# Kernel optimization log

Measured on AMD Instinct MI355X. Metric: run time of the kernel, lower is better.

Reference implementation:

```python
import jax, jax.numpy as jnp
import numpy as np

B, T, C, H, W = 4, 5, 512, 32, 32   # bt = B*T = 20
G = 32                              # GroupNorm groups
EPS = 1e-6


def group_norm(x, gamma, beta):
    # x: [N, C, H, W]; normalize per (group-channels, H, W)
    n, c, h, w = x.shape
    xg = x.reshape(n, G, c // G, h * w)
    mu = jnp.mean(xg, axis=(2, 3), keepdims=True)
    var = jnp.mean((xg - mu) ** 2, axis=(2, 3), keepdims=True)
    xn = ((xg - mu) * jax.lax.rsqrt(var + EPS)).reshape(n, c, h, w)
    return xn * gamma[None, :, None, None] + beta[None, :, None, None]


def conv1x1(x, w, b):
    # 1x1 conv == channel matmul. x: [N,C,H,W], w: [O,C], b: [O]
    return jnp.einsum('nchw,oc->nohw', x, w) + b[None, :, None, None]


def setup_inputs() -> dict:
    key = jax.random.key(0)
    ks = jax.random.split(key, 9)
    inp = {'x': jax.random.normal(ks[0], (B * T, C, H, W), jnp.float32)}
    for i, nm in enumerate(['wq', 'wk', 'wv', 'wo', 'wqt', 'wkt', 'wvt', 'wot']):
        inp[nm] = jax.random.normal(ks[i + 1], (C, C), jnp.float32) * 0.02
        inp['b' + nm[1:]] = jnp.zeros((C,), jnp.float32)
    inp['gamma_s'] = jnp.ones((C,), jnp.float32)
    inp['beta_s'] = jnp.zeros((C,), jnp.float32)
    inp['gamma_t'] = jnp.ones((C,), jnp.float32)
    inp['beta_t'] = jnp.zeros((C,), jnp.float32)
    return inp


def reference(x, wq, bq, wk, bk, wv, bv, wo, bo,
              wqt, bqt, wkt, bkt, wvt, bvt, wot, bot,
              gamma_s, beta_s, gamma_t, beta_t):
    scale = float(C) ** -0.5

    # ---- spatial attention (AttnBlock.forward) ----
    hn = group_norm(x, gamma_s, beta_s)
    q = conv1x1(hn, wq, bq).reshape(B * T, C, H * W)
    k = conv1x1(hn, wk, bk).reshape(B * T, C, H * W)
    v = conv1x1(hn, wv, bv).reshape(B * T, C, H * W)
    # scores [bt, hw_q, hw_k], softmax over keys
    att = jax.nn.softmax(jnp.einsum('bcq,bck->bqk', q, k) * scale, axis=2)
    hsp = jnp.einsum('bck,bqk->bcq', v, att).reshape(B * T, C, H, W)
    spatio = x + conv1x1(hsp, wo, bo)

    # ---- temporal attention across t=5 frames per pixel ----
    hn = group_norm(spatio, gamma_t, beta_t)
    q5 = conv1x1(hn, wqt, bqt).reshape(B, T, C, H, W)
    k5 = conv1x1(hn, wkt, bkt).reshape(B, T, C, H, W)
    v5 = conv1x1(hn, wvt, bvt).reshape(B, T, C, H, W)
    # per-pixel [t, t] attention, softmax over key-frame axis s
    att_t = jax.nn.softmax(jnp.einsum('btchw,bschw->bhwts', q5, k5) * scale, axis=-1)
    htp = jnp.einsum('bhwts,bschw->btchw', att_t, v5).reshape(B * T, C, H, W)

    # NOTE: residual is the ORIGINAL x (faithful to the source), not spatio
    return x + conv1x1(htp, wot, bot)
```

## Files before the change

### kernel.cpp

```cpp
#include <hip/hip_runtime.h>
#include <hip/hip_bf16.h>
#include <stdint.h>

typedef unsigned short u16;
typedef __attribute__((ext_vector_type(8))) short bf16x8;
typedef __attribute__((ext_vector_type(4))) float f32x4;

#define DI __device__ __forceinline__

DI float b2f(u16 u) { return __uint_as_float(((uint32_t)u) << 16); }
DI u16 f2b(float f) {
  uint32_t u = __float_as_uint(f);
  u += 0x7fff + ((u >> 16) & 1);
  return (u16)(u >> 16);
}

DI void gld_lds16(const u16* g, u16* l) {
  __builtin_amdgcn_global_load_lds((const __attribute__((address_space(1))) void*)g,
                                   (__attribute__((address_space(3))) void*)l,
                                   16, 0, 0);
}

__global__ __launch_bounds__(256)
void setup_wb(const float* __restrict__ w0, const float* __restrict__ w1,
              const float* __restrict__ w2, const float* __restrict__ w3,
              const float* __restrict__ w4, const float* __restrict__ w5,
              const float* __restrict__ w6, const float* __restrict__ w7,
              const float* __restrict__ b0, const float* __restrict__ b1,
              const float* __restrict__ b2, const float* __restrict__ b3,
              const float* __restrict__ b4, const float* __restrict__ b5,
              const float* __restrict__ b6, const float* __restrict__ b7,
              u16* __restrict__ dst, float* __restrict__ bdst)
{
  if (blockIdx.x >= 1024) {
    const float* bs[8] = {b0, b1, b2, b3, b4, b5, b6, b7};
    const int a = blockIdx.x - 1024;
    const int i = threadIdx.x;
    bdst[a * 512 + i] = bs[a][i];
    bdst[a * 512 + i + 256] = bs[a][i + 256];
    return;
  }
  const float* srcs[8] = {w0, w1, w2, w3, w4, w5, w6, w7};
  const int mat = blockIdx.x >> 7;
  const int i = (((blockIdx.x & 127) << 8) + threadIdx.x) * 8;
  const float* s = srcs[mat];
  float4 a = *(const float4*)(s + i);
  float4 b = *(const float4*)(s + i + 4);
  alignas(16) u16 v[8] = {f2b(a.x), f2b(a.y), f2b(a.z), f2b(a.w),
                          f2b(b.x), f2b(b.y), f2b(b.z), f2b(b.w)};
  *(uint4*)(dst + (long)mat * 262144 + i) = *(const uint4*)v;
}

template<int OUTF32, int BIASMODE, int RESID>
__global__ __launch_bounds__(512, 2)
void gemm256(const u16* __restrict__ A, long sA, long lda,
             const u16* __restrict__ B, long sB, long ldb,
             void* __restrict__ C, long sC,
             const float* __restrict__ bias,
             const float* __restrict__ resid, long sR,
             int N, int K, float alpha)
{
  __shared__ u16 lA[4 * 8192];
  __shared__ u16 lB[4 * 8192];
  const int t = threadIdx.x;
  const int lane = t & 63, wid = t >> 6;
  const int wr = wid >> 2, wc = wid & 3;
  const int ml = lane & 15, qd = lane >> 4;

  const int nx = gridDim.x;
  const int bid = blockIdx.y * nx + blockIdx.x;
  const int nper = (nx * gridDim.y) >> 3;
  const int nid = (bid & 7) * nper + (bid >> 3);
  const int m0 = (nid / nx) * 256, n0 = (nid % nx) * 256;

  const long bz = blockIdx.z;
  const u16* Ab = A + bz * sA;
  const u16* Bb = B + bz * sB;

  const int sw = ((lane & 3) ^ ((lane >> 3) & 3)) << 3;
  const int srow = wid * 32 + (lane >> 2);
  const u16* ApS = Ab + (long)(m0 + srow) * lda + sw;
  const u16* BpS = Bb + (long)(n0 + srow) * ldb + sw;
  u16* lwA = lA + wid * 1024;
  u16* lwB = lB + wid * 1024;

  f32x4 acc[8][4];
#pragma unroll
  for (int i = 0; i < 8; ++i)
#pragma unroll
    for (int j = 0; j < 4; ++j) acc[i][j] = (f32x4){0.f, 0.f, 0.f, 0.f};

  const int NT = K >> 5;

  auto stageA = [&](int tk) {
    const int bo = (tk & 3) << 13;
    const u16* p = ApS + ((long)tk << 5);
    gld_lds16(p,              lwA + bo);
    gld_lds16(p + (lda << 4), lwA + bo + 512);
  };
  auto stageB = [&](int tk) {
    const int bo = (tk & 3) << 13;
    const u16* p = BpS + ((long)tk << 5);
    gld_lds16(p,              lwB + bo);
    gld_lds16(p + (ldb << 4), lwB + bo + 512);
  };

  const int koff = (qd ^ ((ml >> 1) & 3)) << 3;
  const int rAo = (wr * 128 + ml) * 32 + koff;
  const int rBo = (wc * 64 + ml) * 32 + koff;

  stageA(0); stageB(0); stageA(1); stageB(1); stageA(2); stageB(2);
  asm volatile("s_waitcnt vmcnt(8)" ::: "memory");
  __builtin_amdgcn_s_barrier();
  __builtin_amdgcn_sched_barrier(0);

  for (int tk = 0; tk < NT; ++tk) {
    const int bo = (tk & 3) << 13;
    const u16* pa = lA + bo + rAo;
    const u16* pb = lB + bo + rBo;
    bf16x8 bfr[4], af[4];

#pragma unroll
    for (int n = 0; n < 4; ++n) bfr[n] = *(const bf16x8*)(pb + n * 512);
#pragma unroll
    for (int m = 0; m < 4; ++m) af[m] = *(const bf16x8*)(pa + m * 512);
    if (tk + 3 < NT) stageA(tk + 3);
    __builtin_amdgcn_sched_barrier(0);
    __builtin_amdgcn_s_barrier();
    asm volatile("s_waitcnt lgkmcnt(0)" ::: "memory");
    __builtin_amdgcn_sched_barrier(0);
    __builtin_amdgcn_s_setprio(1);
#pragma unroll
    for (int m = 0; m < 4; ++m)
#pragma unroll
      for (int n = 0; n < 4; ++n)
        acc[m][n] = __builtin_amdgcn_mfma_f32_16x16x32_bf16(af[m], bfr[n], acc[m][n], 0, 0, 0);
    __builtin_amdgcn_s_setprio(0);
    __builtin_amdgcn_sched_barrier(0);
    __builtin_amdgcn_s_barrier();
    __builtin_amdgcn_sched_barrier(0);

#pragma unroll
    for (int m = 0; m < 4; ++m) af[m] = *(const bf16x8*)(pa + (m + 4) * 512);
    if (tk + 3 < NT) stageB(tk + 3);
    __builtin_amdgcn_sched_barrier(0);
    __builtin_amdgcn_s_barrier();
    asm volatile("s_waitcnt lgkmcnt(0)" ::: "memory");
    __builtin_amdgcn_sched_barrier(0);
    __builtin_amdgcn_s_setprio(1);
#pragma unroll
    for (int m = 0; m < 4; ++m)
#pragma unroll
      for (int n = 0; n < 4; ++n)
        acc[m + 4][n] = __builtin_amdgcn_mfma_f32_16x16x32_bf16(af[m], bfr[n], acc[m + 4][n], 0, 0, 0);
    __builtin_amdgcn_s_setprio(0);
    __builtin_amdgcn_sched_barrier(0);

    if (tk < NT - 1) {
      const int rem = NT - 2 - tk;
      if (rem >= 2)      asm volatile("s_waitcnt vmcnt(8)" ::: "memory");
      else if (rem == 1) asm volatile("s_waitcnt vmcnt(4)" ::: "memory");
      else               asm volatile("s_waitcnt vmcnt(0)" ::: "memory");
      __builtin_amdgcn_s_barrier();
      __builtin_amdgcn_sched_barrier(0);
    }
  }

  const long cb = bz * sC;
#pragma unroll
  for (int mt = 0; mt < 8; ++mt) {
#pragma unroll
    for (int nt = 0; nt < 4; ++nt) {
#pragma unroll
      for (int r = 0; r < 4; ++r) {
        int rr = m0 + wr * 128 + mt * 16 + qd * 4 + r;
        int cc = n0 + wc * 64 + nt * 16 + ml;
        float v = acc[mt][nt][r] * alpha;
        if (BIASMODE == 1) v += bias[rr];
        if (BIASMODE == 2) v += bias[cc];
        long idx = (long)rr * N + cc;
        if (RESID) v += resid[bz * sR + idx];
        if (OUTF32) ((float*)C)[cb + idx] = v;
        else        ((u16*)C)[cb + idx] = f2b(v);
      }
    }
  }
}

__global__ __launch_bounds__(256)
void groupnorm_f32(const float* __restrict__ x, const float* __restrict__ gamma,
                   const float* __restrict__ beta, u16* __restrict__ out)
{
  const int C = 512, HW = 1024;
  const int n = blockIdx.x >> 5, g = blockIdx.x & 31;
  const float* xg = x + ((long)n * C + g * 16) * HW;
  const int t = threadIdx.x;
  float s = 0.f, ss = 0.f;
  for (int ch = t; ch < 4096; ch += 256) {
    float4 u = *(const float4*)(xg + ch * 4);
    s += u.x + u.y + u.z + u.w;
    ss += u.x * u.x + u.y * u.y + u.z * u.z + u.w * u.w;
  }
#pragma unroll
  for (int off = 32; off > 0; off >>= 1) { s += __shfl_xor(s, off); ss += __shfl_xor(ss, off); }
  __shared__ float rs[4], rss[4];
  if ((t & 63) == 0) { rs[t >> 6] = s; rss[t >> 6] = ss; }
  __syncthreads();
  s  = rs[0] + rs[1] + rs[2] + rs[3];
  ss = rss[0] + rss[1] + rss[2] + rss[3];
  const float mu = s * (1.f / 16384.f);
  const float var = ss * (1.f / 16384.f) - mu * mu;
  const float rstd = rsqrtf(var + 1e-6f);
  float gm[16], bt[16];
#pragma unroll
  for (int i = 0; i < 16; ++i) {
    float ga = gamma[g * 16 + i];
    gm[i] = ga * rstd;
    bt[i] = beta[g * 16 + i] - mu * ga * rstd;
  }
  for (int p = t; p < 1024; p += 256) {
    alignas(16) u16 vals[16];
#pragma unroll
    for (int i = 0; i < 16; ++i)
      vals[i] = f2b(xg[(long)i * HW + p] * gm[i] + bt[i]);
    u16* dst = out + ((long)n * HW + p) * C + g * 16;
    *(uint4*)dst       = *(const uint4*)&vals[0];
    *(uint4*)(dst + 8) = *(const uint4*)&vals[8];
  }
}

__global__ __launch_bounds__(256)
void groupnorm_bf16(const u16* __restrict__ x, const float* __restrict__ gamma,
                    const float* __restrict__ beta, u16* __restrict__ out)
{
  const int C = 512, HW = 1024;
  const int n = blockIdx.x >> 5, g = blockIdx.x & 31;
  const u16* xg = x + ((long)n * C + g * 16) * HW;
  const int t = threadIdx.x;
  float s = 0.f, ss = 0.f;
  for (int ch = t; ch < 2048; ch += 256) {
    uint4 u = *(const uint4*)(xg + ch * 8);
    uint32_t w[4] = {u.x, u.y, u.z, u.w};
#pragma unroll
    for (int k = 0; k < 4; ++k) {
      float f0 = __uint_as_float(w[k] << 16);
      float f1 = __uint_as_float(w[k] & 0xffff0000u);
      s += f0 + f1; ss += f0 * f0 + f1 * f1;
    }
  }
#pragma unroll
  for (int off = 32; off > 0; off >>= 1) { s += __shfl_xor(s, off); ss += __shfl_xor(ss, off); }
  __shared__ float rs[4], rss[4];
  if ((t & 63) == 0) { rs[t >> 6] = s; rss[t >> 6] = ss; }
  __syncthreads();
  s  = rs[0] + rs[1] + rs[2] + rs[3];
  ss = rss[0] + rss[1] + rss[2] + rss[3];
  const float mu = s * (1.f / 16384.f);
  const float var = ss * (1.f / 16384.f) - mu * mu;
  const float rstd = rsqrtf(var + 1e-6f);
  float gm[16], bt[16];
#pragma unroll
  for (int i = 0; i < 16; ++i) {
    float ga = gamma[g * 16 + i];
    gm[i] = ga * rstd;
    bt[i] = beta[g * 16 + i] - mu * ga * rstd;
  }
  for (int p = t; p < 1024; p += 256) {
    alignas(16) u16 vals[16];
#pragma unroll
    for (int i = 0; i < 16; ++i)
      vals[i] = f2b(b2f(xg[(long)i * HW + p]) * gm[i] + bt[i]);
    u16* dst = out + ((long)n * HW + p) * C + g * 16;
    *(uint4*)dst       = *(const uint4*)&vals[0];
    *(uint4*)(dst + 8) = *(const uint4*)&vals[8];
  }
}

__global__ __launch_bounds__(256)
void softmax1024(u16* __restrict__ data)
{
  u16* row = data + (long)blockIdx.x * 1024;
  const int t = threadIdx.x;
  uint2 u = *(const uint2*)(row + t * 4);
  float v[4];
  v[0] = __uint_as_float(u.x << 16); v[1] = __uint_as_float(u.x & 0xffff0000u);
  v[2] = __uint_as_float(u.y << 16); v[3] = __uint_as_float(u.y & 0xffff0000u);
  float mx = fmaxf(fmaxf(v[0], v[1]), fmaxf(v[2], v[3]));
#pragma unroll
  for (int off = 32; off > 0; off >>= 1) mx = fmaxf(mx, __shfl_xor(mx, off));
  __shared__ float red[8];
  if ((t & 63) == 0) red[t >> 6] = mx;
  __syncthreads();
  mx = fmaxf(fmaxf(red[0], red[1]), fmaxf(red[2], red[3]));
  float e[4]; float s = 0.f;
#pragma unroll
  for (int k = 0; k < 4; ++k) { e[k] = __expf(v[k] - mx); s += e[k]; }
#pragma unroll
  for (int off = 32; off > 0; off >>= 1) s += __shfl_xor(s, off);
  if ((t & 63) == 0) red[4 + (t >> 6)] = s;
  __syncthreads();
  s = red[4] + red[5] + red[6] + red[7];
  float inv = 1.f / s;
  uint2 o;
  o.x = (uint32_t)f2b(e[0] * inv) | ((uint32_t)f2b(e[1] * inv) << 16);
  o.y = (uint32_t)f2b(e[2] * inv) | ((uint32_t)f2b(e[3] * inv) << 16);
  *(uint2*)(row + t * 4) = o;
}

__global__ __launch_bounds__(256)
void temporal_attn(const u16* __restrict__ qkv, u16* __restrict__ htp)
{
  const int t = threadIdx.x;
  const int wv = t >> 6, lane = t & 63;
  const int pix = blockIdx.x * 4 + wv;
  const int b = pix >> 10, p = pix & 1023;
  const long fs = 1024l * 1536;
  const long rowbase = ((long)b * 5 * 1024 + p) * 1536 + lane * 8;

  float qf[5][8], kf[5][8];
#pragma unroll
  for (int f = 0; f < 5; ++f) {
    bf16x8 qv = *(const bf16x8*)(qkv + rowbase + f * fs);
    bf16x8 kv = *(const bf16x8*)(qkv + rowbase + f * fs + 512);
#pragma unroll
    for (int u = 0; u < 8; ++u) { qf[f][u] = b2f((u16)qv[u]); kf[f][u] = b2f((u16)kv[u]); }
  }
  float sc[25];
#pragma unroll
  for (int i = 0; i < 5; ++i)
#pragma unroll
    for (int j = 0; j < 5; ++j) {
      float a = 0.f;
#pragma unroll
      for (int u = 0; u < 8; ++u) a += qf[i][u] * kf[j][u];
      sc[i * 5 + j] = a;
    }
#pragma unroll
  for (int m = 1; m < 64; m <<= 1)
#pragma unroll
    for (int s = 0; s < 25; ++s) sc[s] += __shfl_xor(sc[s], m);

  const float scale = 0.04419417382415922f;
  float att[5][5];
#pragma unroll
  for (int i = 0; i < 5; ++i) {
    float m = sc[i * 5];
#pragma unroll
    for (int j = 1; j < 5; ++j) m = fmaxf(m, sc[i * 5 + j]);
    float ssum = 0.f;
#pragma unroll
    for (int j = 0; j < 5; ++j) { att[i][j] = __expf((sc[i * 5 + j] - m) * scale); ssum += att[i][j]; }
    float inv = 1.f / ssum;
#pragma unroll
    for (int j = 0; j < 5; ++j) att[i][j] *= inv;
  }

  float of[5][8];
#pragma unroll
  for (int i = 0; i < 5; ++i)
#pragma unroll
    for (int u = 0; u < 8; ++u) of[i][u] = 0.f;
#pragma unroll
  for (int s = 0; s < 5; ++s) {
    bf16x8 vvv = *(const bf16x8*)(qkv + rowbase + s * fs + 1024);
#pragma unroll
    for (int u = 0; u < 8; ++u) {
      float vf = b2f((u16)vvv[u]);
#pragma unroll
      for (int i = 0; i < 5; ++i) of[i][u] += att[i][s] * vf;
    }
  }
  const long obase = ((long)b * 5 * 1024 + p) * 512 + lane * 8;
#pragma unroll
  for (int i = 0; i < 5; ++i) {
    alignas(16) u16 ob[8];
#pragma unroll
    for (int u = 0; u < 8; ++u) ob[u] = f2b(of[i][u]);
    *(uint4*)(htp + obase + i * 1024 * 512) = *(const uint4*)ob;
  }
}

extern "C" void kernel_launch(void* const* d_in, const int* in_sizes, int n_in,
                              void* d_out, int out_size, void* d_ws, size_t ws_size,
                              hipStream_t stream)
{
  const float* x   = (const float*)d_in[0];
  const float* wq  = (const float*)d_in[1];
  const float* bq  = (const float*)d_in[2];
  const float* wk  = (const float*)d_in[3];
  const float* bk  = (const float*)d_in[4];
  const float* wv  = (const float*)d_in[5];
  const float* bv  = (const float*)d_in[6];
  const float* wo  = (const float*)d_in[7];
  const float* bo  = (const float*)d_in[8];
  const float* wqt = (const float*)d_in[9];
  const float* bqt = (const float*)d_in[10];
  const float* wkt = (const float*)d_in[11];
  const float* bkt = (const float*)d_in[12];
  const float* wvt = (const float*)d_in[13];
  const float* bvt = (const float*)d_in[14];
  const float* wot = (const float*)d_in[15];
  const float* bot = (const float*)d_in[16];
  const float* gs  = (const float*)d_in[17];
  const float* bs  = (const float*)d_in[18];
  const float* gt  = (const float*)d_in[19];
  const float* btt = (const float*)d_in[20];

  const long U = 20l * 1024 * 512;
  u16* W0 = (u16*)d_ws;
  u16* W1 = W0 + U;
  u16* W3 = W0 + 3 * U;
  u16* W4 = W0 + 4 * U;
  u16* W6 = W0 + 6 * U;
  u16* W7 = W0 + 7 * U;
  u16* Wt = W0 + 8 * U;
  float* Bf = (float*)(Wt + 8 * 262144);
  u16* wv_b  = Wt + 2 * 262144;
  u16* wo_b  = Wt + 3 * 262144;
  u16* wqt_b = Wt + 4 * 262144;
  u16* wot_b = Wt + 7 * 262144;

  const long S  = 524288;
  const long S2 = 1048576;
  const float scale = 0.04419417382415922f;
  dim3 blk(256);
  dim3 blk5(512);

  setup_wb<<<1032, blk, 0, stream>>>(wq, wk, wv, wo, wqt, wkt, wvt, wot,
                                     bq, bk, bv, bo, bqt, bkt, bvt, bot, Wt, Bf);

  groupnorm_f32<<<640, blk, 0, stream>>>(x, gs, bs, W0);
  gemm256<0, 2, 0><<<dim3(4, 80, 1), blk5, 0, stream>>>(
      W0, 0, 512, Wt, 0, 512, W1, 0, Bf, nullptr, 0, 1024, 512, 1.f);
  gemm256<0, 1, 0><<<dim3(4, 2, 20), blk5, 0, stream>>>(
      wv_b, 0, 512, W0, S, 512, W3, S, Bf + 1024, nullptr, 0, 1024, 512, 1.f);
  gemm256<0, 0, 0><<<dim3(4, 4, 20), blk5, 0, stream>>>(
      W1, S2, 1024, W1 + 512, S2, 1024, W4, S2, nullptr, nullptr, 0, 1024, 512, scale);
  softmax1024<<<20480, blk, 0, stream>>>(W4);
  gemm256<0, 0, 0><<<dim3(2, 4, 20), blk5, 0, stream>>>(
      W4, S2, 1024, W3, S, 1024, W0, S, nullptr, nullptr, 0, 512, 1024, 1.f);
  gemm256<0, 1, 1><<<dim3(4, 2, 20), blk5, 0, stream>>>(
      wo_b, 0, 512, W0, S, 512, W6, S, Bf + 1536, x, S, 1024, 512, 1.f);
  groupnorm_bf16<<<640, blk, 0, stream>>>(W6, gt, btt, W7);
  gemm256<0, 2, 0><<<dim3(6, 80, 1), blk5, 0, stream>>>(
      W7, 0, 512, wqt_b, 0, 512, W1, 0, Bf + 2048, nullptr, 0, 1536, 512, 1.f);
  temporal_attn<<<1024, blk, 0, stream>>>(W1, W0);
  gemm256<1, 1, 1><<<dim3(4, 2, 20), blk5, 0, stream>>>(
      wot_b, 0, 512, W0, S, 512, (float*)d_out, S, Bf + 3584, x, S, 1024, 512, 1.f);
}
```

Baseline: 459.1 us.

## Fold output projection into value weights and add 128x128 bf16 GEMM kernel

Precomputes Wo·Wv (and Wo·bv as a fused bias) so the spatial attention output projection is absorbed into the V projection. This removes one per-frame GEMM and lets attention·V write straight into the residual output with bias and x added. It also adds a smaller 128x128-tile, 256-thread GEMM kernel with XCD-aware block remapping and uses it for most GEMMs in place of the 256-tile kernel. The folded weights are rounded to bf16 after the product, which changes rounding slightly, and setup gains a scalar bias matvec and a transposed copy of Wv.

After: 458.2 us. No clear change (-0.2%).

```diff
diff --git a/kernel.cpp b/kernel.cpp
--- a/kernel.cpp
+++ b/kernel.cpp
@@ -32,6 +32,13 @@
               const float* __restrict__ b6, const float* __restrict__ b7,
               u16* __restrict__ dst, float* __restrict__ bdst)
 {
+  if (blockIdx.x >= 1032) {
+    const int a = (blockIdx.x - 1032) * 256 + threadIdx.x;
+    float acc = 0.f;
+    for (int c = 0; c < 512; ++c) acc += w3[a * 512 + c] * b2[c];
+    bdst[4096 + a] = acc;
+    return;
+  }
   if (blockIdx.x >= 1024) {
     const float* bs[8] = {b0, b1, b2, b3, b4, b5, b6, b7};
     const int a = blockIdx.x - 1024;
@@ -49,6 +56,102 @@
   alignas(16) u16 v[8] = {f2b(a.x), f2b(a.y), f2b(a.z), f2b(a.w),
                           f2b(b.x), f2b(b.y), f2b(b.z), f2b(b.w)};
   *(uint4*)(dst + (long)mat * 262144 + i) = *(const uint4*)v;
+  if (mat == 2) {
+    const int row = i >> 9, col = i & 511;
+#pragma unroll
+    for (int j = 0; j < 8; ++j) dst[8 * 262144 + (col + j) * 512 + row] = v[j];
+  }
+}
+
+template<int OUTF32, int BIASMODE, int RESID>
+__global__ __launch_bounds__(256)
+void gemm_bt(const u16* __restrict__ A, long sA, long lda,
+             const u16* __restrict__ B, long sB, long ldb,
+             void* __restrict__ C, long sC,
+             const float* __restrict__ bias,
+             const float* __restrict__ resid, long sR,
+             int N, int K, float alpha)
+{
+  __shared__ u16 lA[2 * 128 * 32];
+  __shared__ u16 lB[2 * 128 * 32];
+  const int t = threadIdx.x;
+  const int lane = t & 63;
+  const int wid = t >> 6;
+
+  const int nx = gridDim.x;
+  const int bid = blockIdx.y * nx + blockIdx.x;
+  const int nper = (nx * gridDim.y) >> 3;
+  const int nid = (bid & 7) * nper + (bid >> 3);
+  const int m0 = (nid / nx) * 128, n0 = (nid % nx) * 128;
+
+  const long bz = blockIdx.z;
+  const u16* Ab = A + bz * sA;
+  const u16* Bb = B + bz * sB;
+
+  const int row = t >> 2;
+  const int kc  = (((t & 3) ^ ((t >> 3) & 3)) << 3);
+
+  f32x4 acc[4][4];
+#pragma unroll
+  for (int i = 0; i < 4; ++i)
+#pragma unroll
+    for (int j = 0; j < 4; ++j) acc[i][j] = (f32x4){0.f, 0.f, 0.f, 0.f};
+
+  const int ml = lane & 15, qd = lane >> 4;
+  const int koff = ((qd ^ ((ml >> 1) & 3)) << 3);
+  const int wm = (wid >> 1) * 64, wn = (wid & 1) * 64;
+
+  auto stage = [&](int bsel, int k0) {
+    const u16* Ap = Ab + (long)(m0 + row) * lda + (k0 + kc);
+    const u16* Bp = Bb + (long)(n0 + row) * ldb + (k0 + kc);
+    u16* la = lA + bsel * 4096 + wid * 512;
+    u16* lb = lB + bsel * 4096 + wid * 512;
+    gld_lds16(Ap, la);
+    gld_lds16(Ap + 64 * lda, la + 2048);
+    gld_lds16(Bp, lb);
+    gld_lds16(Bp + 64 * ldb, lb + 2048);
+  };
+
+  const int niter = K >> 5;
+  stage(0, 0);
+  for (int i = 0; i < niter; ++i) {
+    __syncthreads();
+    if (i + 1 < niter) stage((i + 1) & 1, (i + 1) << 5);
+    const u16* la = lA + (i & 1) * 4096;
+    const u16* lb = lB + (i & 1) * 4096;
+    bf16x8 af[4], bfr[4];
+#pragma unroll
+    for (int x = 0; x < 4; ++x)
+      af[x] = *(const bf16x8*)&la[(wm + x * 16 + ml) * 32 + koff];
+#pragma unroll
+    for (int y = 0; y < 4; ++y)
+      bfr[y] = *(const bf16x8*)&lb[(wn + y * 16 + ml) * 32 + koff];
+#pragma unroll
+    for (int x = 0; x < 4; ++x)
+#pragma unroll
+      for (int y = 0; y < 4; ++y)
+        acc[x][y] = __builtin_amdgcn_mfma_f32_16x16x32_bf16(af[x], bfr[y], acc[x][y], 0, 0, 0);
+  }
+
+  const long cb = bz * sC;
+#pragma unroll
+  for (int i = 0; i < 4; ++i) {
+#pragma unroll
+    for (int j = 0; j < 4; ++j) {
+#pragma unroll
+      for (int r = 0; r < 4; ++r) {
+        int rr = m0 + wm + i * 16 + qd * 4 + r;
+        int cc = n0 + wn + j * 16 + ml;
+        float v = acc[i][j][r] * alpha;
+        if (BIASMODE == 1) v += bias[rr];
+        if (BIASMODE == 2) v += bias[cc];
+        long idx = (long)rr * N + cc;
+        if (RESID) v += resid[bz * sR + idx];
+        if (OUTF32) ((float*)C)[cb + idx] = v;
+        else        ((u16*)C)[cb + idx] = f2b(v);
+      }
+    }
+  }
 }
 
 template<int OUTF32, int BIASMODE, int RESID>
@@ -414,8 +517,9 @@
   u16* W6 = W0 + 6 * U;
   u16* W7 = W0 + 7 * U;
   u16* Wt = W0 + 8 * U;
-  float* Bf = (float*)(Wt + 8 * 262144);
-  u16* wv_b  = Wt + 2 * 262144;
+  u16* wvT_b = Wt + 8 * 262144;
+  u16* Wovs  = Wt + 9 * 262144;
+  float* Bf = (float*)(Wt + 10 * 262144);
   u16* wo_b  = Wt + 3 * 262144;
   u16* wqt_b = Wt + 4 * 262144;
   u16* wot_b = Wt + 7 * 262144;
@@ -426,25 +530,26 @@
   dim3 blk(256);
   dim3 blk5(512);
 
-  setup_wb<<<1032, blk, 0, stream>>>(wq, wk, wv, wo, wqt, wkt, wvt, wot,
+  setup_wb<<<1034, blk, 0, stream>>>(wq, wk, wv, wo, wqt, wkt, wvt, wot,
                                      bq, bk, bv, bo, bqt, bkt, bvt, bot, Wt, Bf);
 
+  gemm_bt<0, 0, 0><<<dim3(4, 4, 1), blk, 0, stream>>>(
+      wo_b, 0, 512, wvT_b, 0, 512, Wovs, 0, nullptr, nullptr, 0, 512, 512, 1.f);
+
   groupnorm_f32<<<640, blk, 0, stream>>>(x, gs, bs, W0);
-  gemm256<0, 2, 0><<<dim3(4, 80, 1), blk5, 0, stream>>>(
+  gemm_bt<0, 2, 0><<<dim3(8, 160, 1), blk, 0, stream>>>(
       W0, 0, 512, Wt, 0, 512, W1, 0, Bf, nullptr, 0, 1024, 512, 1.f);
-  gemm256<0, 1, 0><<<dim3(4, 2, 20), blk5, 0, stream>>>(
-      wv_b, 0, 512, W0, S, 512, W3, S, Bf + 1024, nullptr, 0, 1024, 512, 1.f);
-  gemm256<0, 0, 0><<<dim3(4, 4, 20), blk5, 0, stream>>>(
+  gemm_bt<0, 1, 0><<<dim3(8, 4, 20), blk, 0, stream>>>(
+      Wovs, 0, 512, W0, S, 512, W3, S, Bf + 4096, nullptr, 0, 1024, 512, 1.f);
+  gemm_bt<0, 0, 0><<<dim3(8, 8, 20), blk, 0, stream>>>(
       W1, S2, 1024, W1 + 512, S2, 1024, W4, S2, nullptr, nullptr, 0, 1024, 512, scale);
   softmax1024<<<20480, blk, 0, stream>>>(W4);
-  gemm256<0, 0, 0><<<dim3(2, 4, 20), blk5, 0, stream>>>(
-      W4, S2, 1024, W3, S, 1024, W0, S, nullptr, nullptr, 0, 512, 1024, 1.f);
-  gemm256<0, 1, 1><<<dim3(4, 2, 20), blk5, 0, stream>>>(
-      wo_b, 0, 512, W0, S, 512, W6, S, Bf + 1536, x, S, 1024, 512, 1.f);
+  gemm_bt<0, 1, 1><<<dim3(8, 4, 20), blk, 0, stream>>>(
+      W3, S, 1024, W4, S2, 1024, W6, S, Bf + 1536, x, S, 1024, 1024, 1.f);
   groupnorm_bf16<<<640, blk, 0, stream>>>(W6, gt, btt, W7);
   gemm256<0, 2, 0><<<dim3(6, 80, 1), blk5, 0, stream>>>(
       W7, 0, 512, wqt_b, 0, 512, W1, 0, Bf + 2048, nullptr, 0, 1536, 512, 1.f);
   temporal_attn<<<1024, blk, 0, stream>>>(W1, W0);
-  gemm256<1, 1, 1><<<dim3(4, 2, 20), blk5, 0, stream>>>(
+  gemm_bt<1, 1, 1><<<dim3(8, 4, 20), blk, 0, stream>>>(
       wot_b, 0, 512, W0, S, 512, (float*)d_out, S, Bf + 3584, x, S, 1024, 512, 1.f);
 }
```
